# Kernel tuning notes

Hardware: AMD Instinct MI355X
Metric: run time of the kernel (lower is better)

The kernel has to match this reference:

```python
import jax, jax.numpy as jnp
import numpy as np

B, S, D, H, HID, NL = 4, 512, 1024, 16, 4096, 2
HD = D // H          # head_dim = 64
NBRANCH = 3          # TA, TV, AV
L = NBRANCH * NL     # total cross-attention layers
LN_EPS = 1e-5


def setup_inputs() -> dict:
    key = jax.random.key(0)
    ks = iter(jax.random.split(key, 32))

    def n(shape, s=0.02):
        return jax.random.normal(next(ks), shape, jnp.float32) * s

    inp = {
        "text_features": jax.random.normal(next(ks), (B, S, D), jnp.float32),
        "audio_features": jax.random.normal(next(ks), (B, S, D), jnp.float32),
        "visual_features": jax.random.normal(next(ks), (B, S, D), jnp.float32),
        # projection weights, stacked over all L = 3*num_layers layers
        "WQ": n((L, D, D)), "bQ": jnp.zeros((L, D), jnp.float32),
        "WK": n((L, D, D)), "bK": jnp.zeros((L, D), jnp.float32),
        "WV1": n((L, D, D)), "bV1": jnp.zeros((L, D), jnp.float32),
        "WV2": n((L, D, D)), "bV2": jnp.zeros((L, D), jnp.float32),
        "WO1": n((L, D, D)), "bO1": jnp.zeros((L, D), jnp.float32),
        "WO2": n((L, D, D)), "bO2": jnp.zeros((L, D), jnp.float32),
        # two FFNs per layer (one per modality branch output)
        "F1W1": n((L, D, HID)), "F1b1": jnp.zeros((L, HID), jnp.float32),
        "F1W2": n((L, HID, D)), "F1b2": jnp.zeros((L, D), jnp.float32),
        "F2W1": n((L, D, HID)), "F2b1": jnp.zeros((L, HID), jnp.float32),
        "F2W2": n((L, HID, D)), "F2b2": jnp.zeros((L, D), jnp.float32),
        # layernorms
        "LN1g": jnp.ones((L, D), jnp.float32), "LN1b": jnp.zeros((L, D), jnp.float32),
        "LN2g": jnp.ones((L, D), jnp.float32), "LN2b": jnp.zeros((L, D), jnp.float32),
    }
    return inp


def _ln(x, g, b):
    m = jnp.mean(x, axis=-1, keepdims=True)
    v = jnp.mean(jnp.square(x - m), axis=-1, keepdims=True)
    return (x - m) * jax.lax.rsqrt(v + LN_EPS) * g + b


def reference(text_features, audio_features, visual_features,
              WQ, bQ, WK, bK, WV1, bV1, WV2, bV2, WO1, bO1, WO2, bO2,
              F1W1, F1b1, F1W2, F1b2, F2W1, F2b1, F2W2, F2b2,
              LN1g, LN1b, LN2g, LN2b):
    scale = 1.0 / np.sqrt(HD)

    def layer(i, m1, m2):
        b, s, d = m1.shape

        def heads(x, W, bias):
            return (x @ W + bias).reshape(b, s, H, HD).transpose(0, 2, 1, 3)  # [B,H,S,HD]

        Q = heads(m1, WQ[i], bQ[i])
        K = heads(m2, WK[i], bK[i])
        V1 = heads(m1, WV1[i], bV1[i])
        V2 = heads(m2, WV2[i], bV2[i])

        S1 = jax.nn.softmax(jnp.einsum('bhqd,bhkd->bhqk', Q, K) * scale, axis=-1)
        S2 = jax.nn.softmax(jnp.einsum('bhqd,bhkd->bhqk', K, Q) * scale, axis=-1)

        nV1 = jnp.einsum('bhqk,bhkd->bhqd', S2, V1).transpose(0, 2, 1, 3).reshape(b, s, d)
        nV2 = jnp.einsum('bhqk,bhkd->bhqd', S1, V2).transpose(0, 2, 1, 3).reshape(b, s, d)

        o1 = nV1 @ WO1[i] + bO1[i] + m1
        o2 = nV2 @ WO2[i] + bO2[i] + m2

        x1 = _ln(o1, LN1g[i], LN1b[i])
        x2 = _ln(o2, LN2g[i], LN2b[i])
        f1 = jax.nn.relu(x1 @ F1W1[i] + F1b1[i]) @ F1W2[i] + F1b2[i]
        f2 = jax.nn.relu(x2 @ F2W1[i] + F2b1[i]) @ F2W2[i] + F2b2[i]
        return o1 + f1, o2 + f2

    def branch(bi, a, c):
        for l in range(NL):
            a, c = layer(bi * NL + l, a, c)
        return a, c

    ta_t, ta_a = branch(0, text_features, audio_features)
    tv_t, tv_v = branch(1, text_features, visual_features)
    av_a, av_v = branch(2, audio_features, visual_features)
    return (ta_t, ta_a, tv_t, tv_v, av_a, av_v)
```

## Files before the change

kernel.cpp:

```cpp
#include <hip/hip_runtime.h>
#include <hip/hip_bf16.h>
#include <stdint.h>

typedef unsigned short u16;
typedef __attribute__((ext_vector_type(8))) short bfrag;
typedef __attribute__((ext_vector_type(4))) float ffrag;

#define BB 4
#define SS 512
#define DD 1024
#define HH 16
#define HID 4096

__device__ __forceinline__ u16 f2b(float f){
  union { float f; uint32_t u; } v; v.f = f;
  uint32_t r = v.u + 0x7FFFu + ((v.u >> 16) & 1u);
  return (u16)(r >> 16);
}

__device__ __forceinline__ void gload_lds16(const void* g, void* l){
  __builtin_amdgcn_global_load_lds(
      (const __attribute__((address_space(1))) uint32_t*)g,
      (__attribute__((address_space(3))) uint32_t*)l, 16, 0, 0);
}

struct GemmArgs {
  const u16*  A[12];
  const u16*  W[12];
  const float* bias[12];
  const float* resid[12];
  float* Cf[12];
  u16*   Cb[12];
  int N, K;
};

template<int EPI, int TN>
__global__ __launch_bounds__(256, 2)
void gemm_kernel(GemmArgs args)
{
  __shared__ u16 As[128*64];
  __shared__ u16 Bs[TN*64];

  const int t = threadIdx.x;
  const int N = args.N, K = args.K;
  const int nbn = N / TN;
  const int tiles = 16 * nbn;
  const int cpx = gridDim.x >> 3;
  const int wg = (blockIdx.x & 7) * cpx + (blockIdx.x >> 3);
  const int g  = wg / tiles;
  const int rem = wg - g * tiles;
  const int bm = rem / nbn, bn = rem - bm * nbn;

  const u16* Ap = args.A[g] + (size_t)(bm * 128) * K;
  const u16* Wp = args.W[g] + (size_t)(bn * TN) * K;

  const int w = t >> 6, l = t & 63;
  const int wm = w >> 1, wn = w & 1;
  const int lr = l & 15, lg = l >> 4;
  constexpr int NF = TN / 32;

  ffrag acc[4][NF];
  const ffrag zero = {0.f,0.f,0.f,0.f};
  #pragma unroll
  for (int i=0;i<4;i++)
    #pragma unroll
    for (int j=0;j<NF;j++) acc[i][j] = zero;

  auto issueA = [&](int kk){
    #pragma unroll
    for (int i=0;i<4;i++){
      int ch = (w << 6) + l + (i << 8);
      int r = ch >> 3, cl = ch & 7;
      int cs = cl ^ (r & 7);
      gload_lds16(Ap + (size_t)r*K + kk + cs*8, As + ch*8);
    }
  };
  auto issueB = [&](int kk){
    constexpr int NCH = (TN * 8) / 256;
    #pragma unroll
    for (int i=0;i<NCH;i++){
      int ch = (w << 6) + l + (i << 8);
      int r = ch >> 3, cl = ch & 7;
      int cs = cl ^ (r & 7);
      gload_lds16(Wp + (size_t)r*K + kk + cs*8, Bs + ch*8);
    }
  };
  auto compute = [&](){
    #pragma unroll
    for (int ks=0; ks<2; ks++){
      bfrag a[4], b[NF];
      const int c = ks*4 + lg;
      #pragma unroll
      for (int fm=0; fm<4; fm++){
        int r = wm*64 + fm*16 + lr;
        a[fm] = *(const bfrag*)((const char*)As + r*128 + ((c ^ (r & 7)) << 4));
      }
      #pragma unroll
      for (int fn=0; fn<NF; fn++){
        int n = wn*(TN/2) + fn*16 + lr;
        b[fn] = *(const bfrag*)((const char*)Bs + n*128 + ((c ^ (n & 7)) << 4));
      }
      #pragma unroll
      for (int fm=0; fm<4; fm++)
        #pragma unroll
        for (int fn=0; fn<NF; fn++)
          acc[fm][fn] = __builtin_amdgcn_mfma_f32_16x16x32_bf16(a[fm], b[fn], acc[fm][fn], 0, 0, 0);
    }
  };

  issueA(0); issueB(0);
  const int nt = K >> 6;
  for (int tt=0; tt<nt; tt++){
    __syncthreads();
    compute();
    __syncthreads();
    if (tt+1 < nt){ issueA((tt+1) << 6); issueB((tt+1) << 6); }
  }

  const float* biasp = args.bias[g];
  const float* residp = args.resid[g];
  float* Cf = args.Cf[g];
  u16*   Cb = args.Cb[g];
  const int row0 = bm*128 + wm*64;
  const int col0 = bn*TN + wn*(TN/2);
  #pragma unroll
  for (int fn=0; fn<NF; fn++){
    int col = col0 + fn*16 + lr;
    float bv = biasp[col];
    #pragma unroll
    for (int fm=0; fm<4; fm++){
      #pragma unroll
      for (int r=0; r<4; r++){
        int row = row0 + fm*16 + lg*4 + r;
        size_t idx = (size_t)row*N + col;
        float v = acc[fm][fn][r] + bv;
        if (EPI == 1) v = fmaxf(v, 0.f);
        if (EPI >= 2) { v += residp[idx]; Cf[idx] = v; }
        if (EPI == 0 || EPI == 1 || EPI == 3) Cb[idx] = f2b(v);
      }
    }
  }
}

struct WcvtArgs { const float* W[18]; u16* Wt[18]; };

__global__ __launch_bounds__(256)
void wcvt_kernel(WcvtArgs args, int K, int N)
{
  __shared__ float tile[64][65];
  const int nbn = N >> 6;
  const int tilesPerSlot = (K >> 6) * nbn;
  const int slot = blockIdx.x / tilesPerSlot;
  const int rem  = blockIdx.x - slot * tilesPerSlot;
  const int k0 = (rem / nbn) << 6, n0 = (rem - (rem / nbn) * nbn) << 6;
  const float* W = args.W[slot];
  u16* Wt = args.Wt[slot];
  const int t = threadIdx.x;
  #pragma unroll
  for (int i=0;i<4;i++){
    int ch = t + (i<<8);
    int r = ch >> 4, c4 = ch & 15;
    float4 v = *(const float4*)(W + (size_t)(k0+r)*N + n0 + c4*4);
    tile[r][c4*4+0] = v.x; tile[r][c4*4+1] = v.y;
    tile[r][c4*4+2] = v.z; tile[r][c4*4+3] = v.w;
  }
  __syncthreads();
  #pragma unroll
  for (int i=0;i<2;i++){
    int ch = t + (i<<8);
    int nr = ch >> 3, kc = ch & 7;
    u16 tmp[8];
    #pragma unroll
    for (int j=0;j<8;j++) tmp[j] = f2b(tile[kc*8+j][nr]);
    *(uint4*)(Wt + (size_t)(n0+nr)*K + k0 + kc*8) = *(const uint4*)tmp;
  }
}

struct FlashArgs {
  const u16* Q[6]; const u16* K[6]; const u16* V[6]; u16* O[6];
};

__global__ __launch_bounds__(256, 3)
void flash_kernel(FlashArgs args)
{
  __shared__ u16 Qs[64*64];
  __shared__ u16 Ks[64*64];
  __shared__ u16 Vt[64*64];
  __shared__ u16 Ps[64*64];

  const int t = threadIdx.x;
  const int cpx = gridDim.x >> 3;
  const int wgid = (blockIdx.x & 7) * cpx + (blockIdx.x >> 3);
  const int slot = wgid >> 9;
  const int rem  = wgid & 511;
  const int bh = rem >> 3, qt = rem & 7;
  const int b = bh >> 4, h = bh & 15;
  const int s0 = qt * 64;

  const u16* Qg = args.Q[slot];
  const u16* Kg = args.K[slot];
  const u16* Vg = args.V[slot];
  u16* Og = args.O[slot];

  const int w = t >> 6, l = t & 63;
  const int lr = l & 15, lg = l >> 4;
  const float SCALE = 0.125f;

  #pragma unroll
  for (int i=0;i<2;i++){
    int ch = (w << 6) + l + (i << 8);
    int r = ch >> 3, cl = ch & 7;
    int cs = cl ^ (r & 7);
    gload_lds16(Qg + ((size_t)(b*SS + s0 + r))*DD + h*64 + cs*8, Qs + ch*8);
  }

  float mprev[4], lsum[4];
  #pragma unroll
  for (int r=0;r<4;r++){ mprev[r] = -INFINITY; lsum[r] = 0.f; }
  ffrag oacc[4];
  const ffrag zero = {0.f,0.f,0.f,0.f};
  #pragma unroll
  for (int i=0;i<4;i++) oacc[i] = zero;

  const int kb = t >> 4, nb = t & 15;
  const int k0 = kb*4, n0 = nb*4;

  for (int kt=0; kt<8; kt++){
    const int ks0 = kt*64;
    #pragma unroll
    for (int i=0;i<2;i++){
      int ch = (w << 6) + l + (i << 8);
      int r = ch >> 3, cl = ch & 7;
      int cs = cl ^ (r & 7);
      gload_lds16(Kg + ((size_t)(b*SS + ks0 + r))*DD + h*64 + cs*8, Ks + ch*8);
    }
    {
      u16 va[4][4];
      #pragma unroll
      for (int i=0;i<4;i++)
        *(uint2*)va[i] = *(const uint2*)(Vg + ((size_t)(b*SS + ks0 + k0 + i))*DD + h*64 + n0);
      #pragma unroll
      for (int j=0;j<4;j++){
        int n = n0 + j;
        ushort4 pk;
        pk.x = va[0][j]; pk.y = va[1][j]; pk.z = va[2][j]; pk.w = va[3][j];
        *(ushort4*)((char*)Vt + n*128 + (((k0>>3) ^ (n&7))<<4) + ((k0&7)<<1)) = pk;
      }
    }
    __syncthreads();

    ffrag sacc[4];
    #pragma unroll
    for (int i=0;i<4;i++) sacc[i] = zero;
    #pragma unroll
    for (int ks=0; ks<2; ks++){
      const int c = ks*4 + lg;
      int rq = w*16 + lr;
      bfrag a = *(const bfrag*)((const char*)Qs + rq*128 + ((c ^ (rq&7))<<4));
      #pragma unroll
      for (int fn=0; fn<4; fn++){
        int rk = fn*16 + lr;
        bfrag bb = *(const bfrag*)((const char*)Ks + rk*128 + ((c ^ (rk&7))<<4));
        sacc[fn] = __builtin_amdgcn_mfma_f32_16x16x32_bf16(a, bb, sacc[fn], 0, 0, 0);
      }
    }

    #pragma unroll
    for (int rr=0; rr<4; rr++){
      float s0v = sacc[0][rr]*SCALE, s1v = sacc[1][rr]*SCALE;
      float s2v = sacc[2][rr]*SCALE, s3v = sacc[3][rr]*SCALE;
      float mx = fmaxf(fmaxf(s0v,s1v), fmaxf(s2v,s3v));
      #pragma unroll
      for (int o=1;o<16;o<<=1) mx = fmaxf(mx, __shfl_xor(mx, o));
      float nm = fmaxf(mprev[rr], mx);
      float fac = __expf(mprev[rr] - nm);
      mprev[rr] = nm;
      float p0 = __expf(s0v - nm), p1 = __expf(s1v - nm);
      float p2 = __expf(s2v - nm), p3 = __expf(s3v - nm);
      float psum = (p0+p1)+(p2+p3);
      #pragma unroll
      for (int o=1;o<16;o<<=1) psum += __shfl_xor(psum, o);
      lsum[rr] = lsum[rr]*fac + psum;
      #pragma unroll
      for (int fn=0; fn<4; fn++) oacc[fn][rr] *= fac;
      int row = w*16 + lg*4 + rr;
      int swz = (row & 7) << 4;
      float pv[4] = {p0,p1,p2,p3};
      #pragma unroll
      for (int fn=0; fn<4; fn++){
        int col = fn*16 + lr;
        int addr = row*128 + ((((col>>3)<<4) ^ swz)) + ((col&7)<<1);
        *(u16*)((char*)Ps + addr) = f2b(pv[fn]);
      }
    }
    __builtin_amdgcn_sched_barrier(0);

    #pragma unroll
    for (int ks=0; ks<2; ks++){
      const int c = ks*4 + lg;
      int rq = w*16 + lr;
      bfrag a = *(const bfrag*)((const char*)Ps + rq*128 + ((c ^ (rq&7))<<4));
      #pragma unroll
      for (int fn=0; fn<4; fn++){
        int n = fn*16 + lr;
        bfrag bb = *(const bfrag*)((const char*)Vt + n*128 + ((c ^ (n&7))<<4));
        oacc[fn] = __builtin_amdgcn_mfma_f32_16x16x32_bf16(a, bb, oacc[fn], 0, 0, 0);
      }
    }
    __syncthreads();
  }

  float inv[4];
  #pragma unroll
  for (int rr=0; rr<4; rr++) inv[rr] = 1.f / lsum[rr];
  #pragma unroll
  for (int fn=0; fn<4; fn++){
    int col = h*64 + fn*16 + lr;
    #pragma unroll
    for (int rr=0; rr<4; rr++){
      int qrow = s0 + w*16 + lg*4 + rr;
      Og[((size_t)(b*SS + qrow))*DD + col] = f2b(oacc[fn][rr] * inv[rr]);
    }
  }
}

struct LnArgs {
  const float* X[6]; const float* g[6]; const float* b[6]; u16* O[6];
};

__device__ __forceinline__ float block_reduce_sum(float v){
  #pragma unroll
  for (int o=32;o;o>>=1) v += __shfl_xor(v,o);
  __shared__ float sm[4];
  if ((threadIdx.x&63)==0) sm[threadIdx.x>>6] = v;
  __syncthreads();
  float r = sm[0]+sm[1]+sm[2]+sm[3];
  __syncthreads();
  return r;
}

__global__ __launch_bounds__(256)
void ln6_kernel(LnArgs args)
{
  const int bi = blockIdx.x >> 11;
  const int row = blockIdx.x & 2047;
  const float* x = args.X[bi] + (size_t)row*DD;
  const int t = threadIdx.x;
  float4 v = ((const float4*)x)[t];
  float mean = block_reduce_sum(v.x+v.y+v.z+v.w) * (1.f/DD);
  float d0=v.x-mean, d1=v.y-mean, d2=v.z-mean, d3=v.w-mean;
  float var = block_reduce_sum(d0*d0+d1*d1+d2*d2+d3*d3) * (1.f/DD);
  float rs = rsqrtf(var + 1e-5f);
  float4 gg = ((const float4*)args.g[bi])[t];
  float4 bb = ((const float4*)args.b[bi])[t];
  ushort4 o;
  o.x = f2b(d0*rs*gg.x + bb.x);
  o.y = f2b(d1*rs*gg.y + bb.y);
  o.z = f2b(d2*rs*gg.z + bb.z);
  o.w = f2b(d3*rs*gg.w + bb.w);
  ((ushort4*)(args.O[bi] + (size_t)row*DD))[t] = o;
}

__global__ __launch_bounds__(256)
void cvt3_kernel(const float* __restrict__ i0, const float* __restrict__ i1,
                 const float* __restrict__ i2, u16* __restrict__ o0,
                 u16* __restrict__ o1, u16* __restrict__ o2)
{
  const int sel = blockIdx.x >> 10;
  const float* in = sel==0 ? i0 : sel==1 ? i1 : i2;
  u16* out = sel==0 ? o0 : sel==1 ? o1 : o2;
  size_t i = (((size_t)(blockIdx.x & 1023))*256 + threadIdx.x)*8;
  float4 a = *(const float4*)(in+i);
  float4 b = *(const float4*)(in+i+4);
  ushort4 q0, q1;
  q0.x=f2b(a.x); q0.y=f2b(a.y); q0.z=f2b(a.z); q0.w=f2b(a.w);
  q1.x=f2b(b.x); q1.y=f2b(b.y); q1.z=f2b(b.z); q1.w=f2b(b.w);
  *(ushort4*)(out+i) = q0;
  *(ushort4*)(out+i+4) = q1;
}

extern "C" void kernel_launch(void* const* d_in, const int* in_sizes, int n_in,
                              void* d_out, int out_size, void* d_ws, size_t ws_size,
                              hipStream_t stream)
{
  (void)in_sizes; (void)n_in; (void)out_size; (void)ws_size;
  const float* text   = (const float*)d_in[0];
  const float* audio  = (const float*)d_in[1];
  const float* visual = (const float*)d_in[2];
  const float* WQ  = (const float*)d_in[3];
  const float* bQ  = (const float*)d_in[4];
  const float* WK  = (const float*)d_in[5];
  const float* bK  = (const float*)d_in[6];
  const float* WV1 = (const float*)d_in[7];
  const float* bV1 = (const float*)d_in[8];
  const float* WV2 = (const float*)d_in[9];
  const float* bV2 = (const float*)d_in[10];
  const float* WO1 = (const float*)d_in[11];
  const float* bO1 = (const float*)d_in[12];
  const float* WO2 = (const float*)d_in[13];
  const float* bO2 = (const float*)d_in[14];
  const float* F1W1 = (const float*)d_in[15];
  const float* F1b1 = (const float*)d_in[16];
  const float* F1W2 = (const float*)d_in[17];
  const float* F1b2 = (const float*)d_in[18];
  const float* F2W1 = (const float*)d_in[19];
  const float* F2b1 = (const float*)d_in[20];
  const float* F2W2 = (const float*)d_in[21];
  const float* F2b2 = (const float*)d_in[22];
  const float* LN1g = (const float*)d_in[23];
  const float* LN1b = (const float*)d_in[24];
  const float* LN2g = (const float*)d_in[25];
  const float* LN2b = (const float*)d_in[26];
  float* outp = (float*)d_out;

  char* ws = (char*)d_ws;
  size_t off = 0;
  auto alloc = [&](size_t bytes)->char*{
    char* p = ws + off; off += (bytes + 255) & ~(size_t)255; return p;
  };
  const size_t NTOK = (size_t)BB*SS;
  const size_t AB = NTOK*DD*2;
  const size_t E  = NTOK*DD;

  u16* inb[3];
  for (int i=0;i<3;i++) inb[i] = (u16*)alloc(AB);
  u16 *Qb[3], *Kb[3], *V1b[3], *V2b[3], *nV1b[3], *nV2b[3];
  for (int i=0;i<3;i++){
    Qb[i]=(u16*)alloc(AB); Kb[i]=(u16*)alloc(AB);
    V1b[i]=(u16*)alloc(AB); V2b[i]=(u16*)alloc(AB);
  }
  for (int i=0;i<3;i++){ nV1b[i]=(u16*)alloc(AB); nV2b[i]=(u16*)alloc(AB); }
  float* Lgp = (float*)alloc((size_t)BB*HH*SS*SS*4);
  u16* P1p   = (u16*)alloc((size_t)BB*HH*SS*SS*2);
  u16* P2Tp  = (u16*)alloc((size_t)BB*HH*SS*SS*2);
  u16* Wtb   = (u16*)alloc((size_t)6*DD*HID*2);

  u16 *x1b[3], *x2b[3], *h1b[3], *h2b[3], *mid1b[3], *mid2b[3];
  for (int i=0;i<3;i++){ x1b[i]=Qb[i]; x2b[i]=Kb[i]; }
  u16* Lgu = (u16*)Lgp;
  h1b[0]=Lgu;        h2b[0]=Lgu+ 4*E;
  h1b[1]=Lgu+8*E;    h2b[1]=Lgu+12*E;
  h1b[2]=P1p;        h2b[2]=P1p+ 4*E;
  for (int i=0;i<3;i++){ mid1b[i]=P2Tp+(size_t)(2*i)*E; mid2b[i]=P2Tp+(size_t)(2*i+1)*E; }

  cvt3_kernel<<<3072,256,0,stream>>>(text, audio, visual, inb[0], inb[1], inb[2]);

  const size_t OSZ = E;
  const size_t DD2 = (size_t)DD*DD;
  const size_t DH = (size_t)DD*HID;
  struct Br { const float* f1; const u16* b1; const float* f2; const u16* b2; int s1, s2; };
  Br brs[3] = {{text,inb[0],audio,inb[1],0,1},{text,inb[0],visual,inb[2],2,3},{audio,inb[1],visual,inb[2],4,5}};

  for (int li=0; li<2; li++){
    const u16* m1b[3]; const u16* m2b[3];
    float* t1f[3]; float* t2f[3];
    for (int bi=0; bi<3; bi++){
      m1b[bi] = li==0 ? brs[bi].b1 : mid1b[bi];
      m2b[bi] = li==0 ? brs[bi].b2 : mid2b[bi];
      t1f[bi] = outp + (size_t)brs[bi].s1*OSZ;
      t2f[bi] = outp + (size_t)brs[bi].s2*OSZ;
    }

    {
      WcvtArgs wa{};
      for (int bi=0; bi<3; bi++){
        const int i = bi*2 + li;
        wa.W[bi*4+0]=WQ +i*DD2; wa.W[bi*4+1]=WK +i*DD2;
        wa.W[bi*4+2]=WV1+i*DD2; wa.W[bi*4+3]=WV2+i*DD2;
        for (int s=0;s<4;s++) wa.Wt[bi*4+s] = Wtb + (size_t)(bi*4+s)*DD2;
        wa.W[12+bi*2+0]=WO1+i*DD2; wa.W[12+bi*2+1]=WO2+i*DD2;
        wa.Wt[12+bi*2+0]=Wtb + (size_t)(12+bi*2+0)*DD2;
        wa.Wt[12+bi*2+1]=Wtb + (size_t)(12+bi*2+1)*DD2;
      }
      wcvt_kernel<<<4608,256,0,stream>>>(wa, DD, DD);
    }
    {
      GemmArgs ga{};
      for (int bi=0; bi<3; bi++){
        const int i = bi*2 + li;
        ga.A[bi*4+0]=m1b[bi]; ga.bias[bi*4+0]=bQ +(size_t)i*DD; ga.Cb[bi*4+0]=Qb[bi];
        ga.A[bi*4+1]=m2b[bi]; ga.bias[bi*4+1]=bK +(size_t)i*DD; ga.Cb[bi*4+1]=Kb[bi];
        ga.A[bi*4+2]=m1b[bi]; ga.bias[bi*4+2]=bV1+(size_t)i*DD; ga.Cb[bi*4+2]=V1b[bi];
        ga.A[bi*4+3]=m2b[bi]; ga.bias[bi*4+3]=bV2+(size_t)i*DD; ga.Cb[bi*4+3]=V2b[bi];
        for (int s=0;s<4;s++) ga.W[bi*4+s] = Wtb + (size_t)(bi*4+s)*DD2;
      }
      ga.N = DD; ga.K = DD;
      gemm_kernel<0,128><<<1536,256,0,stream>>>(ga);
    }
    {
      FlashArgs fa{};
      for (int bi=0; bi<3; bi++){
        fa.Q[bi*2+0]=Qb[bi]; fa.K[bi*2+0]=Kb[bi]; fa.V[bi*2+0]=V2b[bi]; fa.O[bi*2+0]=nV2b[bi];
        fa.Q[bi*2+1]=Kb[bi]; fa.K[bi*2+1]=Qb[bi]; fa.V[bi*2+1]=V1b[bi]; fa.O[bi*2+1]=nV1b[bi];
      }
      flash_kernel<<<3072,256,0,stream>>>(fa);
    }
    {
      GemmArgs ga{};
      for (int bi=0; bi<3; bi++){
        const int i = bi*2 + li;
        ga.A[bi*2+0]=nV1b[bi]; ga.bias[bi*2+0]=bO1+(size_t)i*DD;
        ga.resid[bi*2+0] = li==0 ? brs[bi].f1 : t1f[bi]; ga.Cf[bi*2+0]=t1f[bi];
        ga.A[bi*2+1]=nV2b[bi]; ga.bias[bi*2+1]=bO2+(size_t)i*DD;
        ga.resid[bi*2+1] = li==0 ? brs[bi].f2 : t2f[bi]; ga.Cf[bi*2+1]=t2f[bi];
        ga.W[bi*2+0]=Wtb + (size_t)(12+bi*2+0)*DD2;
        ga.W[bi*2+1]=Wtb + (size_t)(12+bi*2+1)*DD2;
      }
      ga.N = DD; ga.K = DD;
      gemm_kernel<2,128><<<768,256,0,stream>>>(ga);
    }
    {
      LnArgs la{};
      for (int bi=0; bi<3; bi++){
        const int i = bi*2 + li;
        la.X[bi*2+0]=t1f[bi]; la.g[bi*2+0]=LN1g+(size_t)i*DD; la.b[bi*2+0]=LN1b+(size_t)i*DD; la.O[bi*2+0]=x1b[bi];
        la.X[bi*2+1]=t2f[bi]; la.g[bi*2+1]=LN2g+(size_t)i*DD; la.b[bi*2+1]=LN2b+(size_t)i*DD; la.O[bi*2+1]=x2b[bi];
      }
      ln6_kernel<<<12288,256,0,stream>>>(la);
    }
    {
      WcvtArgs wa{};
      for (int bi=0; bi<3; bi++){
        const int i = bi*2 + li;
        wa.W[bi*2+0]=F1W1+(size_t)i*DH; wa.W[bi*2+1]=F2W1+(size_t)i*DH;
        wa.Wt[bi*2+0]=Wtb + (size_t)(bi*2+0)*DH;
        wa.Wt[bi*2+1]=Wtb + (size_t)(bi*2+1)*DH;
      }
      wcvt_kernel<<<6144,256,0,stream>>>(wa, DD, HID);
      GemmArgs ga{};
      for (int bi=0; bi<3; bi++){
        const int i = bi*2 + li;
        ga.A[bi*2+0]=x1b[bi]; ga.bias[bi*2+0]=F1b1+(size_t)i*HID; ga.Cb[bi*2+0]=h1b[bi];
        ga.A[bi*2+1]=x2b[bi]; ga.bias[bi*2+1]=F2b1+(size_t)i*HID; ga.Cb[bi*2+1]=h2b[bi];
        ga.W[bi*2+0]=Wtb + (size_t)(bi*2+0)*DH;
        ga.W[bi*2+1]=Wtb + (size_t)(bi*2+1)*DH;
      }
      ga.N = HID; ga.K = DD;
      gemm_kernel<1,128><<<3072,256,0,stream>>>(ga);
    }
    {
      WcvtArgs wa{};
      for (int bi=0; bi<3; bi++){
        const int i = bi*2 + li;
        wa.W[bi*2+0]=F1W2+(size_t)i*DH; wa.W[bi*2+1]=F2W2+(size_t)i*DH;
        wa.Wt[bi*2+0]=Wtb + (size_t)(bi*2+0)*DH;
        wa.Wt[bi*2+1]=Wtb + (size_t)(bi*2+1)*DH;
      }
      wcvt_kernel<<<6144,256,0,stream>>>(wa, HID, DD);
      GemmArgs ga{};
      for (int bi=0; bi<3; bi++){
        const int i = bi*2 + li;
        ga.A[bi*2+0]=h1b[bi]; ga.bias[bi*2+0]=F1b2+(size_t)i*DD;
        ga.resid[bi*2+0]=t1f[bi]; ga.Cf[bi*2+0]=t1f[bi]; ga.Cb[bi*2+0]=mid1b[bi];
        ga.A[bi*2+1]=h2b[bi]; ga.bias[bi*2+1]=F2b2+(size_t)i*DD;
        ga.resid[bi*2+1]=t2f[bi]; ga.Cf[bi*2+1]=t2f[bi]; ga.Cb[bi*2+1]=mid2b[bi];
        ga.W[bi*2+0]=Wtb + (size_t)(bi*2+0)*DH;
        ga.W[bi*2+1]=Wtb + (size_t)(bi*2+1)*DH;
      }
      ga.N = DD; ga.K = HID;
      if (li == 0) gemm_kernel<3,128><<<768,256,0,stream>>>(ga);
      else         gemm_kernel<2,128><<<768,256,0,stream>>>(ga);
    }
  }
}
```

Measured before the change: 1.235 ms.

## Add 256x256-tile double-buffered GEMM kernel for FFN up-projection

Adds a new bf16 MFMA GEMM kernel with 256x256 output tiles, 512 threads, XOR-swizzled LDS, direct global-to-LDS loads with a two-stage double buffer, and an XCD-aware block remap. It replaces the 128-tile GEMM only for the first FFN matmul, which has a fused ReLU and bias epilogue. Larger tiles increase data reuse per load and cut global traffic. In exchange, the kernel needs 128KB of LDS and many accumulator registers, which may limit occupancy, and it launches only 768 blocks.

After: 1.256 ms. No clear change (+1.7%).

```diff
diff --git a/kernel.cpp b/kernel.cpp
--- a/kernel.cpp
+++ b/kernel.cpp
@@ -137,6 +137,125 @@
         if (EPI == 1) v = fmaxf(v, 0.f);
         if (EPI >= 2) { v += residp[idx]; Cf[idx] = v; }
         if (EPI == 0 || EPI == 1 || EPI == 3) Cb[idx] = f2b(v);
+      }
+    }
+  }
+}
+
+struct Gemm256Args {
+  const u16* A[6]; const u16* W[6]; const float* bias[6]; u16* Cb[6];
+  int N, K;
+};
+
+__global__ __launch_bounds__(512, 2)
+void gemm256_kernel(Gemm256Args args)
+{
+  __shared__ u16 As[2][256*64];
+  __shared__ u16 Bs[2][256*64];
+
+  const int t = threadIdx.x;
+  const int N = args.N, K = args.K;
+  const int nbn = N >> 8;
+  const int tiles = 8 * nbn;
+  const int cpx = gridDim.x >> 3;
+  const int wg = (blockIdx.x & 7) * cpx + (blockIdx.x >> 3);
+  const int g  = wg / tiles;
+  const int rem = wg - g * tiles;
+  const int bm = rem / nbn, bn = rem - bm * nbn;
+
+  const u16* Ap = args.A[g] + (size_t)(bm * 256) * K;
+  const u16* Wp = args.W[g] + (size_t)(bn * 256) * K;
+
+  const int wid = t >> 6, l = t & 63;
+  const int wm = wid >> 2, wn = wid & 3;
+  const int lr = l & 15, lg = l >> 4;
+
+  ffrag acc[8][4];
+  const ffrag zero = {0.f,0.f,0.f,0.f};
+  #pragma unroll
+  for (int i=0;i<8;i++)
+    #pragma unroll
+    for (int j=0;j<4;j++) acc[i][j] = zero;
+
+  auto stage = [&](int kk, int buf){
+    #pragma unroll
+    for (int i=0;i<4;i++){
+      int ch = (wid << 6) + l + (i << 9);
+      int r = ch >> 3, cl = ch & 7;
+      int cs = cl ^ (r & 7);
+      gload_lds16(Ap + (size_t)r*K + kk + cs*8, As[buf] + ch*8);
+    }
+    #pragma unroll
+    for (int i=0;i<4;i++){
+      int ch = (wid << 6) + l + (i << 9);
+      int r = ch >> 3, cl = ch & 7;
+      int cs = cl ^ (r & 7);
+      gload_lds16(Wp + (size_t)r*K + kk + cs*8, Bs[buf] + ch*8);
+    }
+  };
+
+  stage(0, 0);
+  stage(64, 1);
+  asm volatile("s_waitcnt vmcnt(8)" ::: "memory");
+  __builtin_amdgcn_s_barrier();
+  __builtin_amdgcn_sched_barrier(0);
+
+  const int nt = K >> 6;
+  for (int tt=0; tt<nt; tt++){
+    const int cur = tt & 1;
+    bfrag a[8][2], b[4][2];
+    #pragma unroll
+    for (int ks=0; ks<2; ks++){
+      const int c = ks*4 + lg;
+      #pragma unroll
+      for (int fm=0; fm<8; fm++){
+        int r = wm*128 + fm*16 + lr;
+        a[fm][ks] = *(const bfrag*)((const char*)As[cur] + r*128 + ((c ^ (r & 7)) << 4));
+      }
+      #pragma unroll
+      for (int fn=0; fn<4; fn++){
+        int n = wn*64 + fn*16 + lr;
+        b[fn][ks] = *(const bfrag*)((const char*)Bs[cur] + n*128 + ((c ^ (n & 7)) << 4));
+      }
+    }
+    asm volatile("s_waitcnt lgkmcnt(0)" ::: "memory");
+    __builtin_amdgcn_sched_barrier(0);
+    __builtin_amdgcn_s_barrier();
+    __builtin_amdgcn_sched_barrier(0);
+    if (tt+2 < nt) stage((tt+2) << 6, cur);
+    __builtin_amdgcn_s_setprio(1);
+    #pragma unroll
+    for (int ks=0; ks<2; ks++)
+      #pragma unroll
+      for (int fm=0; fm<8; fm++)
+        #pragma unroll
+        for (int fn=0; fn<4; fn++)
+          acc[fm][fn] = __builtin_amdgcn_mfma_f32_16x16x32_bf16(a[fm][ks], b[fn][ks], acc[fm][fn], 0, 0, 0);
+    __builtin_amdgcn_s_setprio(0);
+    if (tt+1 < nt){
+      if (tt+2 < nt) asm volatile("s_waitcnt vmcnt(8)" ::: "memory");
+      else           asm volatile("s_waitcnt vmcnt(0)" ::: "memory");
+      __builtin_amdgcn_sched_barrier(0);
+      __builtin_amdgcn_s_barrier();
+      __builtin_amdgcn_sched_barrier(0);
+    }
+  }
+
+  const float* biasp = args.bias[g];
+  u16* Cb = args.Cb[g];
+  const int row0 = bm*256 + wm*128;
+  const int col0 = bn*256 + wn*64;
+  #pragma unroll
+  for (int fn=0; fn<4; fn++){
+    int col = col0 + fn*16 + lr;
+    float bv = biasp[col];
+    #pragma unroll
+    for (int fm=0; fm<8; fm++){
+      #pragma unroll
+      for (int r=0; r<4; r++){
+        int row = row0 + fm*16 + lg*4 + r;
+        float v = fmaxf(acc[fm][fn][r] + bv, 0.f);
+        Cb[(size_t)row*N + col] = f2b(v);
       }
     }
   }
@@ -527,7 +646,7 @@
         wa.Wt[bi*2+1]=Wtb + (size_t)(bi*2+1)*DH;
       }
       wcvt_kernel<<<6144,256,0,stream>>>(wa, DD, HID);
-      GemmArgs ga{};
+      Gemm256Args ga{};
       for (int bi=0; bi<3; bi++){
         const int i = bi*2 + li;
         ga.A[bi*2+0]=x1b[bi]; ga.bias[bi*2+0]=F1b1+(size_t)i*HID; ga.Cb[bi*2+0]=h1b[bi];
@@ -536,7 +655,7 @@
         ga.W[bi*2+1]=Wtb + (size_t)(bi*2+1)*DH;
       }
       ga.N = HID; ga.K = DD;
-      gemm_kernel<1,128><<<3072,256,0,stream>>>(ga);
+      gemm256_kernel<<<768,512,0,stream>>>(ga);
     }
     {
       WcvtArgs wa{};
```
